# Optimization experiments

Measured on AMD Instinct MI355X. Metric: run time of the kernel, lower is better.

Reference implementation:

```python
import jax, jax.numpy as jnp
import numpy as np
from jax import lax

KQ = 3  # kernel_size_q
KK = 3  # kernel_size_k
PAD_Q = KQ - 1          # causal (left-only) padding along query dim
PAD_K = (KK - 1) // 2   # centered padding along key dim
CAUSAL = True


def setup_inputs() -> dict:
    key = jax.random.key(0)
    kq, kk, kv, kc = jax.random.split(key, 4)
    B, H, S, D = 1, 16, 2048, 128
    Q = jax.random.normal(kq, (B, H, S, D), dtype=jnp.float32)
    K = jax.random.normal(kk, (B, H, S, D), dtype=jnp.float32)
    V = jax.random.normal(kv, (B, H, S, D), dtype=jnp.float32)
    # module init: normal(mean=0, std=0.2)
    conv_kernel = 0.2 * jax.random.normal(kc, (H, KQ, KK), dtype=jnp.float32)
    return {"Q": Q, "K": K, "V": V, "conv_kernel": conv_kernel}


def reference(Q, K, V, conv_kernel):
    B, H, S, D = Q.shape
    scale = 1.0 / (D ** 0.5)
    # raw attention scores [B, H, Sq, Sk]
    scores = jnp.einsum('bhqd,bhkd->bhqk', Q, K) * scale
    causal_mask = jnp.tril(jnp.ones((S, S), dtype=bool))  # [Sq, Sk]
    if CAUSAL:
        # zero out future positions BEFORE the conv so the kernel cannot leak
        # future keys through the centered key-dim padding
        scores = jnp.where(causal_mask, scores, 0.0)
    # per-head 2D conv over the score matrix (grouped conv, one filter per head).
    # query dim padded only on the left (pad_q = KQ-1) -> each output row mixes
    # the current and previous KQ-1 query rows; key dim padded symmetrically.
    kernel = conv_kernel[:, None, :, :]  # [H, 1, KQ, KK] OIHW
    conv_scores = lax.conv_general_dilated(
        scores, kernel,
        window_strides=(1, 1),
        padding=[(PAD_Q, 0), (PAD_K, PAD_K)],
        dimension_numbers=('NCHW', 'OIHW', 'NCHW'),
        feature_group_count=H,
    )
    if CAUSAL:
        conv_scores = jnp.where(causal_mask, conv_scores, -jnp.inf)
    probs = jax.nn.softmax(conv_scores, axis=-1)
    out = jnp.einsum('bhqk,bhkd->bhqd', probs, V)
    return out
```

## Files before the change

kernel.cpp:

```cpp
#include <hip/hip_runtime.h>
#include <hip/hip_bf16.h>
#include <math.h>

#define S_LEN 2048
#define DIM   128
#define NHEAD 16
#define BQ    62
#define BK    64
#define SCALE 0.08838834764831845f

typedef __attribute__((ext_vector_type(8))) short bf16x8;
typedef __attribute__((ext_vector_type(4))) float f32x4;
typedef __attribute__((ext_vector_type(2))) float f32x2;

__device__ __forceinline__ short f2bf(float f) {
  union { float f; unsigned u; } v; v.f = f;
  unsigned r = v.u + 0x7fffu + ((v.u >> 16) & 1u);
  return (short)(r >> 16);
}
__device__ __forceinline__ float bhi(unsigned u) {
  union { unsigned v; float f; } x; x.v = u & 0xffff0000u; return x.f;
}
__device__ __forceinline__ float blo(unsigned u) {
  union { unsigned v; float f; } x; x.v = u << 16; return x.f;
}
__device__ __forceinline__ float b2f(short s) {
  union { unsigned v; float f; } x; x.v = ((unsigned)(unsigned short)s) << 16; return x.f;
}
__device__ __forceinline__ unsigned cvtpk(float lo, float hi) {
  unsigned r;
  asm("v_cvt_pk_bf16_f32 %0, %1, %2" : "=v"(r) : "v"(lo), "v"(hi));
  return r;
}
__device__ __forceinline__ f32x2 pkfma(f32x2 a, f32x2 b, f32x2 c) {
  f32x2 d;
  asm("v_pk_fma_f32 %0, %1, %2, %3" : "=v"(d) : "v"(a), "v"(b), "v"(c));
  return d;
}
__device__ __forceinline__ void gll16(const void* gsrc, void* ldst) {
  __builtin_amdgcn_global_load_lds(
      (const __attribute__((address_space(1))) void*)gsrc,
      (__attribute__((address_space(3))) void*)ldst, 16, 0, 0);
}

__global__ __launch_bounds__(256)
void prep_k(const float* __restrict__ K, short* __restrict__ Kb) {
  int gid = blockIdx.x * 256 + threadIdx.x;
  int chunk = gid & 15;
  int row = gid >> 4;
  int k = row & (S_LEN - 1);
  const float* src = K + (size_t)row * DIM + chunk * 8;
  float4 a = *(const float4*)(src);
  float4 b = *(const float4*)(src + 4);
  bf16x8 o;
  o[0]=f2bf(a.x*SCALE); o[1]=f2bf(a.y*SCALE); o[2]=f2bf(a.z*SCALE); o[3]=f2bf(a.w*SCALE);
  o[4]=f2bf(b.x*SCALE); o[5]=f2bf(b.y*SCALE); o[6]=f2bf(b.z*SCALE); o[7]=f2bf(b.w*SCALE);
  int cp = (chunk & 8) | ((chunk & 7) ^ (k & 7));
  *(bf16x8*)(Kb + (size_t)row * DIM + cp * 8) = o;
}

__global__ __launch_bounds__(256)
void prep_v(const float* __restrict__ V, short* __restrict__ Vw) {
  __shared__ __align__(16) short lv[128][72];
  int tile = blockIdx.x, h = blockIdx.y;
  const float* src = V + ((size_t)h * S_LEN + tile * 64) * DIM;
  int kr = threadIdx.x >> 2, dq = (threadIdx.x & 3) * 32;
  const float* sp = src + (size_t)kr * DIM + dq;
  #pragma unroll
  for (int j = 0; j < 32; j += 4) {
    float4 v = *(const float4*)(sp + j);
    lv[dq + j][kr]     = f2bf(v.x);
    lv[dq + j + 1][kr] = f2bf(v.y);
    lv[dq + j + 2][kr] = f2bf(v.z);
    lv[dq + j + 3][kr] = f2bf(v.w);
  }
  __syncthreads();
  int d = threadIdx.x >> 1, cbase = (threadIdx.x & 1) * 4;
  short* dst = Vw + ((size_t)h * 32 + tile) * 8192 + (size_t)d * 64;
  #pragma unroll
  for (int c0 = 0; c0 < 4; ++c0) {
    int c = cbase + c0;
    bf16x8 val = *(const bf16x8*)&lv[d][c * 8];
    *(bf16x8*)(dst + ((c ^ (d & 7)) * 8)) = val;
  }
}

__global__ __launch_bounds__(256, 2)
void convattn_main(const float* __restrict__ Q, const short* __restrict__ Kb,
                   const short* __restrict__ Vw, const float* __restrict__ W,
                   float* __restrict__ Out) {
  __shared__ __align__(16) short Kt2[2][64][128];
  __shared__ __align__(16) short Vt[128][64];
  __shared__ __align__(16) short rawS16[2][64][66];
  __shared__ short haloL16[2][64];

  const int bx = blockIdx.x;
  const int rank = (bx < 256) ? bx : ((bx < 512) ? (767 - bx) : bx);
  const int qt = 33 - (rank >> 4);
  const int h  = rank & 15;
  const int q0 = qt * BQ;
  const int qr0 = q0 - 2;
  const int q_cap = min(q0 + BQ - 1, S_LEN - 1);
  const int T = q_cap / BK + 1;

  const int tid  = threadIdx.x;
  const int wid  = tid >> 6;
  const int lane = tid & 63;
  const int lm   = lane & 15;
  const int lg   = lane >> 4;

  const float* Qh = Q + (size_t)h * S_LEN * DIM;
  const short* KbH = Kb + (size_t)h * S_LEN * DIM;
  const short* VwH = Vw + (size_t)h * 32 * 8192;
  float* Oh = Out + (size_t)h * S_LEN * DIM;

  f32x2 wp[9];
  #pragma unroll
  for (int i = 0; i < 9; ++i) { float w = W[h * 9 + i]; wp[i][0] = w; wp[i][1] = w; }

  bf16x8 qf[4];
  {
    int qrow = qr0 + wid * 16 + lm;
    int qc = qrow < 0 ? 0 : (qrow >= S_LEN ? S_LEN - 1 : qrow);
    const float* qp = Qh + (size_t)qc * DIM;
    #pragma unroll
    for (int kk = 0; kk < 4; ++kk) {
      int d0 = kk * 32 + lg * 8;
      float4 a = *(const float4*)(qp + d0);
      float4 b = *(const float4*)(qp + d0 + 4);
      bf16x8 f;
      f[0]=f2bf(a.x); f[1]=f2bf(a.y); f[2]=f2bf(a.z); f[3]=f2bf(a.w);
      f[4]=f2bf(b.x); f[5]=f2bf(b.y); f[6]=f2bf(b.z); f[7]=f2bf(b.w);
      qf[kk] = f;
    }
  }
  if (tid < 64) haloL16[0][tid] = 0;

  float m_state = -INFINITY, l_state = 0.f;
  f32x4 oacc[8];
  const f32x4 zero4 = {0.f, 0.f, 0.f, 0.f};
  #pragma unroll
  for (int cb = 0; cb < 8; ++cb) oacc[cb] = zero4;

  __builtin_amdgcn_sched_barrier(0);
  asm volatile("s_waitcnt vmcnt(0)" ::: "memory");
  {
    const char* vg = (const char*)VwH;
    const char* kg = (const char*)KbH;
    char* vl = (char*)&Vt[0][0];
    char* kl = (char*)&Kt2[0][0][0];
    #pragma unroll
    for (int i = 0; i < 4; ++i) {
      int off = wid * 4096 + i * 1024;
      gll16(vg + off + lane * 16, vl + off);
    }
    #pragma unroll
    for (int i = 0; i < 4; ++i) {
      int off = wid * 4096 + i * 1024;
      gll16(kg + off + lane * 16, kl + off);
    }
  }

  for (int t = 0; t <= T; ++t) {
    asm volatile("s_waitcnt lgkmcnt(0)" ::: "memory");
    __builtin_amdgcn_sched_barrier(0);
    __builtin_amdgcn_s_barrier();
    {
      int vsrc = t > 0 ? t - 1 : 0;
      int ksrc = (t + 1 < T) ? t + 1 : T - 1;
      const char* vg = (const char*)(VwH + (size_t)vsrc * 8192);
      const char* kg = (const char*)(KbH + (size_t)ksrc * BK * DIM);
      char* vl = (char*)&Vt[0][0];
      char* kl = (char*)&Kt2[(t + 1) & 1][0][0];
      #pragma unroll
      for (int i = 0; i < 4; ++i) {
        int off = wid * 4096 + i * 1024;
        gll16(vg + off + lane * 16, vl + off);
      }
      #pragma unroll
      for (int i = 0; i < 4; ++i) {
        int off = wid * 4096 + i * 1024;
        gll16(kg + off + lane * 16, kl + off);
      }
    }
    asm volatile("s_waitcnt vmcnt(8)" ::: "memory");
    __builtin_amdgcn_sched_barrier(0);
    __builtin_amdgcn_s_barrier();
    if (t < T) {
      const short(*Ktile)[128] = Kt2[t & 1];
      int k0 = t * BK;
      f32x4 sacc[4];
      #pragma unroll
      for (int cb = 0; cb < 4; ++cb) sacc[cb] = zero4;
      #pragma unroll
      for (int kk = 0; kk < 4; ++kk) {
        #pragma unroll
        for (int cb = 0; cb < 4; ++cb) {
          int c = kk * 4 + lg;
          int cp = (c & 8) | ((c & 7) ^ (lm & 7));
          bf16x8 bf = *(const bf16x8*)((const char*)&Ktile[cb * 16 + lm][0] + cp * 16);
          sacc[cb] = __builtin_amdgcn_mfma_f32_16x16x32_bf16(qf[kk], bf, sacc[cb], 0, 0, 0);
        }
      }
      const int buf = t & 1;
      #pragma unroll
      for (int cb = 0; cb < 4; ++cb) {
        int rr = wid * 16 + lg * 4;
        int cc = cb * 16 + lm;
        #pragma unroll
        for (int i = 0; i < 4; i += 2) {
          float v0 = ((k0 + cc) <= (qr0 + rr + i))     ? sacc[cb][i]     : 0.f;
          float v1 = ((k0 + cc) <= (qr0 + rr + i + 1)) ? sacc[cb][i + 1] : 0.f;
          unsigned pk = cvtpk(v0, v1);
          rawS16[buf][rr + i][cc]     = (short)pk;
          rawS16[buf][rr + i + 1][cc] = (short)(pk >> 16);
        }
      }
    }
    asm volatile("s_waitcnt vmcnt(4) lgkmcnt(0)" ::: "memory");
    __builtin_amdgcn_sched_barrier(0);
    __builtin_amdgcn_s_barrier();
    if (t > 0) {
      const int tp = t - 1;
      const int pb = tp & 1, nb = pb ^ 1;
      const int c0p = tp * BK;
      const bool haveRight = (t < T);
      const int r = wid * 16 + lm;
      const int q = qr0 + r;
      const bool rowvalid = (r >= 2) && (q <= q_cap);
      const int a0 = max(r - 2, 0), a1 = max(r - 1, 0);
      const short* rp[3] = { &rawS16[pb][a0][0], &rawS16[pb][a1][0], &rawS16[pb][r][0] };
      const int ridx[3] = { a0, a1, r };
      const int cs0 = lg * 8;
      const int cs1 = 32 + lg * 8;
      const bool leftEdge  = (lg == 0);
      const bool rightEdge = (lg == 3);
      const int cA = leftEdge ? 0 : cs0 - 2;

      f32x2 xv[3][10];
      #pragma unroll
      for (int rw = 0; rw < 3; ++rw) {
        const short* p = rp[rw];
        unsigned a0w = *(const unsigned*)(p + cA);
        unsigned a1w = *(const unsigned*)(p + cs0);
        unsigned a2w = *(const unsigned*)(p + cs0 + 2);
        unsigned a3w = *(const unsigned*)(p + cs0 + 4);
        unsigned a4w = *(const unsigned*)(p + cs0 + 6);
        unsigned a5w = *(const unsigned*)(p + cs0 + 8);
        unsigned b0w = *(const unsigned*)(p + cs1 - 2);
        unsigned b1w = *(const unsigned*)(p + cs1);
        unsigned b2w = *(const unsigned*)(p + cs1 + 2);
        unsigned b3w = *(const unsigned*)(p + cs1 + 4);
        unsigned b4w = *(const unsigned*)(p + cs1 + 6);
        unsigned b5w = *(const unsigned*)(p + cs1 + 8);
        float hv = b2f(haloL16[pb][ridx[rw]]);
        float rv = haveRight ? b2f(rawS16[nb][ridx[rw]][0]) : 0.f;
        xv[rw][0][0] = leftEdge ? hv : bhi(a0w);  xv[rw][0][1] = bhi(b0w);
        xv[rw][1][0] = blo(a1w);  xv[rw][1][1] = blo(b1w);
        xv[rw][2][0] = bhi(a1w);  xv[rw][2][1] = bhi(b1w);
        xv[rw][3][0] = blo(a2w);  xv[rw][3][1] = blo(b2w);
        xv[rw][4][0] = bhi(a2w);  xv[rw][4][1] = bhi(b2w);
        xv[rw][5][0] = blo(a3w);  xv[rw][5][1] = blo(b3w);
        xv[rw][6][0] = bhi(a3w);  xv[rw][6][1] = bhi(b3w);
        xv[rw][7][0] = blo(a4w);  xv[rw][7][1] = blo(b4w);
        xv[rw][8][0] = bhi(a4w);  xv[rw][8][1] = bhi(b4w);
        xv[rw][9][0] = blo(a5w);  xv[rw][9][1] = rightEdge ? rv : blo(b5w);
      }

      const int thr0 = rowvalid ? (q - c0p - cs0) : -1;
      const int thr1 = rowvalid ? (q - c0p - cs1) : -1;
      float svx[8], svy[8];
      float pm = -INFINITY;
      #pragma unroll
      for (int c = 0; c < 8; ++c) {
        f32x2 acc = {0.f, 0.f};
        acc = pkfma(wp[0], xv[0][c],     acc);
        acc = pkfma(wp[1], xv[0][c + 1], acc);
        acc = pkfma(wp[2], xv[0][c + 2], acc);
        acc = pkfma(wp[3], xv[1][c],     acc);
        acc = pkfma(wp[4], xv[1][c + 1], acc);
        acc = pkfma(wp[5], xv[1][c + 2], acc);
        acc = pkfma(wp[6], xv[2][c],     acc);
        acc = pkfma(wp[7], xv[2][c + 1], acc);
        acc = pkfma(wp[8], xv[2][c + 2], acc);
        svx[c] = (c <= thr0) ? acc[0] : -INFINITY;
        svy[c] = (c <= thr1) ? acc[1] : -INFINITY;
        pm = fmaxf(pm, fmaxf(svx[c], svy[c]));
      }
      pm = fmaxf(pm, __shfl_xor(pm, 16));
      pm = fmaxf(pm, __shfl_xor(pm, 32));
      const float mn = fmaxf(m_state, pm);
      const float al = __expf(m_state - mn);
      float ps = 0.f;
      union { bf16x8 v; unsigned u[4]; } pf0u, pf1u;
      #pragma unroll
      for (int c = 0; c < 8; c += 2) {
        float p0 = __expf(svx[c] - mn);
        float p1 = __expf(svx[c + 1] - mn);
        float p2 = __expf(svy[c] - mn);
        float p3 = __expf(svy[c + 1] - mn);
        ps += (p0 + p1) + (p2 + p3);
        pf0u.u[c >> 1] = cvtpk(p0, p1);
        pf1u.u[c >> 1] = cvtpk(p2, p3);
      }
      ps += __shfl_xor(ps, 16);
      ps += __shfl_xor(ps, 32);
      m_state = mn;
      l_state = al * l_state + ps;
      if (lg == 0) haloL16[t & 1][r] = rawS16[pb][r][63];
      #pragma unroll
      for (int i = 0; i < 4; ++i) {
        float a = __shfl(al, lg * 4 + i);
        #pragma unroll
        for (int cb = 0; cb < 8; ++cb) oacc[cb][i] *= a;
      }
      #pragma unroll
      for (int kk = 0; kk < 2; ++kk) {
        bf16x8 pf = kk ? pf1u.v : pf0u.v;
        #pragma unroll
        for (int cb = 0; cb < 8; ++cb) {
          int d = cb * 16 + lm;
          int cp = (kk * 4 + lg) ^ (lm & 7);
          bf16x8 vf = *(const bf16x8*)((const char*)&Vt[d][0] + cp * 16);
          oacc[cb] = __builtin_amdgcn_mfma_f32_16x16x32_bf16(pf, vf, oacc[cb], 0, 0, 0);
        }
      }
    }
  }

  asm volatile("s_waitcnt vmcnt(0)" ::: "memory");

  #pragma unroll
  for (int i = 0; i < 4; ++i) {
    int rr = wid * 16 + lg * 4 + i;
    int q = qr0 + rr;
    float lr = __shfl(l_state, lg * 4 + i);
    if (rr >= 2 && q <= q_cap) {
      float inv = 1.f / lr;
      #pragma unroll
      for (int cb = 0; cb < 8; ++cb) {
        Oh[(size_t)q * DIM + cb * 16 + lm] = oacc[cb][i] * inv;
      }
    }
  }
}

extern "C" void kernel_launch(void* const* d_in, const int* in_sizes, int n_in,
                              void* d_out, int out_size, void* d_ws, size_t ws_size,
                              hipStream_t stream) {
  const float* Q = (const float*)d_in[0];
  const float* K = (const float*)d_in[1];
  const float* V = (const float*)d_in[2];
  const float* W = (const float*)d_in[3];
  float* Out = (float*)d_out;
  short* Kb = (short*)d_ws;
  short* Vw = (short*)((char*)d_ws + (size_t)NHEAD * S_LEN * DIM * 2);

  prep_k<<<dim3(NHEAD * S_LEN * 16 / 256), 256, 0, stream>>>(K, Kb);
  prep_v<<<dim3(32, NHEAD), 256, 0, stream>>>(V, Vw);

  convattn_main<<<dim3(544), 256, 0, stream>>>(Q, Kb, Vw, W, Out);
}
```

Before: 104.2 us.

## Read K and V MFMA fragments directly from global memory instead of LDS staging

Removes the async global-to-LDS double-buffered staging of K and V tiles and the XOR swizzles in the prep kernels. The MFMA operands are now loaded straight from global (L2/L1-cached) bf16 buffers, and the custom waitcnt/barrier pipeline becomes plain __syncthreads. LDS use drops, and launch bounds are raised to 4 blocks per SM for more occupancy. The cost is that the tile loads are no longer overlapped with compute through prefetch, and every wave rereads K and V from global memory.

New measurement: 263.0 us. 152% more time.

```diff
diff --git a/kernel.cpp b/kernel.cpp
--- a/kernel.cpp
+++ b/kernel.cpp
@@ -37,26 +37,19 @@
   asm("v_pk_fma_f32 %0, %1, %2, %3" : "=v"(d) : "v"(a), "v"(b), "v"(c));
   return d;
 }
-__device__ __forceinline__ void gll16(const void* gsrc, void* ldst) {
-  __builtin_amdgcn_global_load_lds(
-      (const __attribute__((address_space(1))) void*)gsrc,
-      (__attribute__((address_space(3))) void*)ldst, 16, 0, 0);
-}
 
 __global__ __launch_bounds__(256)
 void prep_k(const float* __restrict__ K, short* __restrict__ Kb) {
   int gid = blockIdx.x * 256 + threadIdx.x;
   int chunk = gid & 15;
   int row = gid >> 4;
-  int k = row & (S_LEN - 1);
   const float* src = K + (size_t)row * DIM + chunk * 8;
   float4 a = *(const float4*)(src);
   float4 b = *(const float4*)(src + 4);
   bf16x8 o;
   o[0]=f2bf(a.x*SCALE); o[1]=f2bf(a.y*SCALE); o[2]=f2bf(a.z*SCALE); o[3]=f2bf(a.w*SCALE);
   o[4]=f2bf(b.x*SCALE); o[5]=f2bf(b.y*SCALE); o[6]=f2bf(b.z*SCALE); o[7]=f2bf(b.w*SCALE);
-  int cp = (chunk & 8) | ((chunk & 7) ^ (k & 7));
-  *(bf16x8*)(Kb + (size_t)row * DIM + cp * 8) = o;
+  *(bf16x8*)(Kb + (size_t)row * DIM + chunk * 8) = o;
 }
 
 __global__ __launch_bounds__(256)
@@ -64,15 +57,15 @@
   __shared__ __align__(16) short lv[128][72];
   int tile = blockIdx.x, h = blockIdx.y;
   const float* src = V + ((size_t)h * S_LEN + tile * 64) * DIM;
-  int kr = threadIdx.x >> 2, dq = (threadIdx.x & 3) * 32;
-  const float* sp = src + (size_t)kr * DIM + dq;
+  int kr = threadIdx.x >> 2, dc = (threadIdx.x & 3) * 32;
+  const float* sp = src + (size_t)kr * DIM + dc;
   #pragma unroll
   for (int j = 0; j < 32; j += 4) {
     float4 v = *(const float4*)(sp + j);
-    lv[dq + j][kr]     = f2bf(v.x);
-    lv[dq + j + 1][kr] = f2bf(v.y);
-    lv[dq + j + 2][kr] = f2bf(v.z);
-    lv[dq + j + 3][kr] = f2bf(v.w);
+    lv[dc + j][kr]     = f2bf(v.x);
+    lv[dc + j + 1][kr] = f2bf(v.y);
+    lv[dc + j + 2][kr] = f2bf(v.z);
+    lv[dc + j + 3][kr] = f2bf(v.w);
   }
   __syncthreads();
   int d = threadIdx.x >> 1, cbase = (threadIdx.x & 1) * 4;
@@ -80,17 +73,14 @@
   #pragma unroll
   for (int c0 = 0; c0 < 4; ++c0) {
     int c = cbase + c0;
-    bf16x8 val = *(const bf16x8*)&lv[d][c * 8];
-    *(bf16x8*)(dst + ((c ^ (d & 7)) * 8)) = val;
-  }
-}
-
-__global__ __launch_bounds__(256, 2)
+    *(bf16x8*)(dst + c * 8) = *(const bf16x8*)&lv[d][c * 8];
+  }
+}
+
+__global__ __launch_bounds__(256, 4)
 void convattn_main(const float* __restrict__ Q, const short* __restrict__ Kb,
-                   const short* __restrict__ Vw, const float* __restrict__ W,
+                   const short* __restrict__ Vw, const float* __restrict__ Wt,
                    float* __restrict__ Out) {
-  __shared__ __align__(16) short Kt2[2][64][128];
-  __shared__ __align__(16) short Vt[128][64];
   __shared__ __align__(16) short rawS16[2][64][66];
   __shared__ short haloL16[2][64];
 
@@ -116,7 +106,7 @@
 
   f32x2 wp[9];
   #pragma unroll
-  for (int i = 0; i < 9; ++i) { float w = W[h * 9 + i]; wp[i][0] = w; wp[i][1] = w; }
+  for (int i = 0; i < 9; ++i) { float w = Wt[h * 9 + i]; wp[i][0] = w; wp[i][1] = w; }
 
   bf16x8 qf[4];
   {
@@ -142,52 +132,9 @@
   #pragma unroll
   for (int cb = 0; cb < 8; ++cb) oacc[cb] = zero4;
 
-  __builtin_amdgcn_sched_barrier(0);
-  asm volatile("s_waitcnt vmcnt(0)" ::: "memory");
-  {
-    const char* vg = (const char*)VwH;
-    const char* kg = (const char*)KbH;
-    char* vl = (char*)&Vt[0][0];
-    char* kl = (char*)&Kt2[0][0][0];
-    #pragma unroll
-    for (int i = 0; i < 4; ++i) {
-      int off = wid * 4096 + i * 1024;
-      gll16(vg + off + lane * 16, vl + off);
-    }
-    #pragma unroll
-    for (int i = 0; i < 4; ++i) {
-      int off = wid * 4096 + i * 1024;
-      gll16(kg + off + lane * 16, kl + off);
-    }
-  }
-
   for (int t = 0; t <= T; ++t) {
-    asm volatile("s_waitcnt lgkmcnt(0)" ::: "memory");
-    __builtin_amdgcn_sched_barrier(0);
-    __builtin_amdgcn_s_barrier();
-    {
-      int vsrc = t > 0 ? t - 1 : 0;
-      int ksrc = (t + 1 < T) ? t + 1 : T - 1;
-      const char* vg = (const char*)(VwH + (size_t)vsrc * 8192);
-      const char* kg = (const char*)(KbH + (size_t)ksrc * BK * DIM);
-      char* vl = (char*)&Vt[0][0];
-      char* kl = (char*)&Kt2[(t + 1) & 1][0][0];
-      #pragma unroll
-      for (int i = 0; i < 4; ++i) {
-        int off = wid * 4096 + i * 1024;
-        gll16(vg + off + lane * 16, vl + off);
-      }
-      #pragma unroll
-      for (int i = 0; i < 4; ++i) {
-        int off = wid * 4096 + i * 1024;
-        gll16(kg + off + lane * 16, kl + off);
-      }
-    }
-    asm volatile("s_waitcnt vmcnt(8)" ::: "memory");
-    __builtin_amdgcn_sched_barrier(0);
-    __builtin_amdgcn_s_barrier();
+    __syncthreads();
     if (t < T) {
-      const short(*Ktile)[128] = Kt2[t & 1];
       int k0 = t * BK;
       f32x4 sacc[4];
       #pragma unroll
@@ -196,9 +143,8 @@
       for (int kk = 0; kk < 4; ++kk) {
         #pragma unroll
         for (int cb = 0; cb < 4; ++cb) {
-          int c = kk * 4 + lg;
-          int cp = (c & 8) | ((c & 7) ^ (lm & 7));
-          bf16x8 bf = *(const bf16x8*)((const char*)&Ktile[cb * 16 + lm][0] + cp * 16);
+          const short* kp = KbH + (size_t)(k0 + cb * 16 + lm) * DIM + (kk * 4 + lg) * 8;
+          bf16x8 bf = *(const bf16x8*)kp;
           sacc[cb] = __builtin_amdgcn_mfma_f32_16x16x32_bf16(qf[kk], bf, sacc[cb], 0, 0, 0);
         }
       }
@@ -217,9 +163,7 @@
         }
       }
     }
-    asm volatile("s_waitcnt vmcnt(4) lgkmcnt(0)" ::: "memory");
-    __builtin_amdgcn_sched_barrier(0);
-    __builtin_amdgcn_s_barrier();
+    __syncthreads();
     if (t > 0) {
       const int tp = t - 1;
       const int pb = tp & 1, nb = pb ^ 1;
@@ -314,21 +258,19 @@
         #pragma unroll
         for (int cb = 0; cb < 8; ++cb) oacc[cb][i] *= a;
       }
+      const short* Vtile = VwH + (size_t)tp * 8192;
       #pragma unroll
       for (int kk = 0; kk < 2; ++kk) {
         bf16x8 pf = kk ? pf1u.v : pf0u.v;
         #pragma unroll
         for (int cb = 0; cb < 8; ++cb) {
-          int d = cb * 16 + lm;
-          int cp = (kk * 4 + lg) ^ (lm & 7);
-          bf16x8 vf = *(const bf16x8*)((const char*)&Vt[d][0] + cp * 16);
+          const short* vp = Vtile + (size_t)(cb * 16 + lm) * 64 + (kk * 4 + lg) * 8;
+          bf16x8 vf = *(const bf16x8*)vp;
           oacc[cb] = __builtin_amdgcn_mfma_f32_16x16x32_bf16(pf, vf, oacc[cb], 0, 0, 0);
         }
       }
     }
   }
-
-  asm volatile("s_waitcnt vmcnt(0)" ::: "memory");
 
   #pragma unroll
   for (int i = 0; i < 4; ++i) {
@@ -353,10 +295,11 @@
   const float* V = (const float*)d_in[2];
   const float* W = (const float*)d_in[3];
   float* Out = (float*)d_out;
+
   short* Kb = (short*)d_ws;
-  short* Vw = (short*)((char*)d_ws + (size_t)NHEAD * S_LEN * DIM * 2);
-
-  prep_k<<<dim3(NHEAD * S_LEN * 16 / 256), 256, 0, stream>>>(K, Kb);
+  short* Vw = (short*)((char*)d_ws + 8388608);
+
+  prep_k<<<dim3(2048), 256, 0, stream>>>(K, Kb);
   prep_v<<<dim3(32, NHEAD), 256, 0, stream>>>(V, Vw);
 
   convattn_main<<<dim3(544), 256, 0, stream>>>(Q, Kb, Vw, W, Out);
```

## Read V fragments directly from global memory and stage fp32 scores in LDS

Applied to the files above, without the earlier changes.

The V tile is no longer staged in LDS through global_load_lds. The PV MFMA B operands are now read straight from the pre-transposed bf16 V workspace in global/L2, and prep_v drops its XOR swizzle to match. The raw score tile is kept in LDS as fp32 with an interleaved column layout instead of packed bf16, so the conv reads float2 pairs directly without unpacking. s_setprio is raised around both MFMA loops. The changes save LDS space and barrier-coupled traffic, but V reads now take per-iteration global latency on the critical path and the LDS score buffer doubles in size.

Result: slower. 159.2 us (+52.7%).

```diff
diff --git a/kernel.cpp b/kernel.cpp
--- a/kernel.cpp
+++ b/kernel.cpp
@@ -17,15 +17,6 @@
   union { float f; unsigned u; } v; v.f = f;
   unsigned r = v.u + 0x7fffu + ((v.u >> 16) & 1u);
   return (short)(r >> 16);
-}
-__device__ __forceinline__ float bhi(unsigned u) {
-  union { unsigned v; float f; } x; x.v = u & 0xffff0000u; return x.f;
-}
-__device__ __forceinline__ float blo(unsigned u) {
-  union { unsigned v; float f; } x; x.v = u << 16; return x.f;
-}
-__device__ __forceinline__ float b2f(short s) {
-  union { unsigned v; float f; } x; x.v = ((unsigned)(unsigned short)s) << 16; return x.f;
 }
 __device__ __forceinline__ unsigned cvtpk(float lo, float hi) {
   unsigned r;
@@ -64,15 +55,15 @@
   __shared__ __align__(16) short lv[128][72];
   int tile = blockIdx.x, h = blockIdx.y;
   const float* src = V + ((size_t)h * S_LEN + tile * 64) * DIM;
-  int kr = threadIdx.x >> 2, dq = (threadIdx.x & 3) * 32;
-  const float* sp = src + (size_t)kr * DIM + dq;
+  int kr = threadIdx.x >> 2, dc = (threadIdx.x & 3) * 32;
+  const float* sp = src + (size_t)kr * DIM + dc;
   #pragma unroll
   for (int j = 0; j < 32; j += 4) {
     float4 v = *(const float4*)(sp + j);
-    lv[dq + j][kr]     = f2bf(v.x);
-    lv[dq + j + 1][kr] = f2bf(v.y);
-    lv[dq + j + 2][kr] = f2bf(v.z);
-    lv[dq + j + 3][kr] = f2bf(v.w);
+    lv[dc + j][kr]     = f2bf(v.x);
+    lv[dc + j + 1][kr] = f2bf(v.y);
+    lv[dc + j + 2][kr] = f2bf(v.z);
+    lv[dc + j + 3][kr] = f2bf(v.w);
   }
   __syncthreads();
   int d = threadIdx.x >> 1, cbase = (threadIdx.x & 1) * 4;
@@ -80,19 +71,17 @@
   #pragma unroll
   for (int c0 = 0; c0 < 4; ++c0) {
     int c = cbase + c0;
-    bf16x8 val = *(const bf16x8*)&lv[d][c * 8];
-    *(bf16x8*)(dst + ((c ^ (d & 7)) * 8)) = val;
+    *(bf16x8*)(dst + c * 8) = *(const bf16x8*)&lv[d][c * 8];
   }
 }
 
 __global__ __launch_bounds__(256, 2)
 void convattn_main(const float* __restrict__ Q, const short* __restrict__ Kb,
-                   const short* __restrict__ Vw, const float* __restrict__ W,
+                   const short* __restrict__ Vw, const float* __restrict__ Wt,
                    float* __restrict__ Out) {
   __shared__ __align__(16) short Kt2[2][64][128];
-  __shared__ __align__(16) short Vt[128][64];
-  __shared__ __align__(16) short rawS16[2][64][66];
-  __shared__ short haloL16[2][64];
+  __shared__ __align__(16) float rawF[2][64][70];
+  __shared__ float haloLF[2][64];
 
   const int bx = blockIdx.x;
   const int rank = (bx < 256) ? bx : ((bx < 512) ? (767 - bx) : bx);
@@ -116,7 +105,7 @@
 
   f32x2 wp[9];
   #pragma unroll
-  for (int i = 0; i < 9; ++i) { float w = W[h * 9 + i]; wp[i][0] = w; wp[i][1] = w; }
+  for (int i = 0; i < 9; ++i) { float w = Wt[h * 9 + i]; wp[i][0] = w; wp[i][1] = w; }
 
   bf16x8 qf[4];
   {
@@ -134,7 +123,7 @@
       qf[kk] = f;
     }
   }
-  if (tid < 64) haloL16[0][tid] = 0;
+  if (tid < 64) haloLF[0][tid] = 0.f;
 
   float m_state = -INFINITY, l_state = 0.f;
   f32x4 oacc[8];
@@ -144,20 +133,12 @@
 
   __builtin_amdgcn_sched_barrier(0);
   asm volatile("s_waitcnt vmcnt(0)" ::: "memory");
+  __builtin_amdgcn_sched_barrier(0);
   {
-    const char* vg = (const char*)VwH;
-    const char* kg = (const char*)KbH;
-    char* vl = (char*)&Vt[0][0];
-    char* kl = (char*)&Kt2[0][0][0];
     #pragma unroll
     for (int i = 0; i < 4; ++i) {
       int off = wid * 4096 + i * 1024;
-      gll16(vg + off + lane * 16, vl + off);
-    }
-    #pragma unroll
-    for (int i = 0; i < 4; ++i) {
-      int off = wid * 4096 + i * 1024;
-      gll16(kg + off + lane * 16, kl + off);
+      gll16((const char*)KbH + off + lane * 16, (char*)&Kt2[0][0][0] + off);
     }
   }
 
@@ -166,24 +147,16 @@
     __builtin_amdgcn_sched_barrier(0);
     __builtin_amdgcn_s_barrier();
     {
-      int vsrc = t > 0 ? t - 1 : 0;
       int ksrc = (t + 1 < T) ? t + 1 : T - 1;
-      const char* vg = (const char*)(VwH + (size_t)vsrc * 8192);
       const char* kg = (const char*)(KbH + (size_t)ksrc * BK * DIM);
-      char* vl = (char*)&Vt[0][0];
       char* kl = (char*)&Kt2[(t + 1) & 1][0][0];
-      #pragma unroll
-      for (int i = 0; i < 4; ++i) {
-        int off = wid * 4096 + i * 1024;
-        gll16(vg + off + lane * 16, vl + off);
-      }
       #pragma unroll
       for (int i = 0; i < 4; ++i) {
         int off = wid * 4096 + i * 1024;
         gll16(kg + off + lane * 16, kl + off);
       }
     }
-    asm volatile("s_waitcnt vmcnt(8)" ::: "memory");
+    asm volatile("s_waitcnt vmcnt(4)" ::: "memory");
     __builtin_amdgcn_sched_barrier(0);
     __builtin_amdgcn_s_barrier();
     if (t < T) {
@@ -192,6 +165,7 @@
       f32x4 sacc[4];
       #pragma unroll
       for (int cb = 0; cb < 4; ++cb) sacc[cb] = zero4;
+      __builtin_amdgcn_s_setprio(1);
       #pragma unroll
       for (int kk = 0; kk < 4; ++kk) {
         #pragma unroll
@@ -202,22 +176,21 @@
           sacc[cb] = __builtin_amdgcn_mfma_f32_16x16x32_bf16(qf[kk], bf, sacc[cb], 0, 0, 0);
         }
       }
+      __builtin_amdgcn_s_setprio(0);
       const int buf = t & 1;
       #pragma unroll
       for (int cb = 0; cb < 4; ++cb) {
         int rr = wid * 16 + lg * 4;
         int cc = cb * 16 + lm;
-        #pragma unroll
-        for (int i = 0; i < 4; i += 2) {
-          float v0 = ((k0 + cc) <= (qr0 + rr + i))     ? sacc[cb][i]     : 0.f;
-          float v1 = ((k0 + cc) <= (qr0 + rr + i + 1)) ? sacc[cb][i + 1] : 0.f;
-          unsigned pk = cvtpk(v0, v1);
-          rawS16[buf][rr + i][cc]     = (short)pk;
-          rawS16[buf][rr + i + 1][cc] = (short)(pk >> 16);
-        }
-      }
-    }
-    asm volatile("s_waitcnt vmcnt(4) lgkmcnt(0)" ::: "memory");
+        int di = ((cc & 31) + 2) * 2 + (cc >> 5);
+        #pragma unroll
+        for (int i = 0; i < 4; ++i) {
+          float v = ((k0 + cc) <= (qr0 + rr + i)) ? sacc[cb][i] : 0.f;
+          rawF[buf][rr + i][di] = v;
+        }
+      }
+    }
+    asm volatile("s_waitcnt lgkmcnt(0)" ::: "memory");
     __builtin_amdgcn_sched_barrier(0);
     __builtin_amdgcn_s_barrier();
     if (t > 0) {
@@ -229,42 +202,34 @@
       const int q = qr0 + r;
       const bool rowvalid = (r >= 2) && (q <= q_cap);
       const int a0 = max(r - 2, 0), a1 = max(r - 1, 0);
-      const short* rp[3] = { &rawS16[pb][a0][0], &rawS16[pb][a1][0], &rawS16[pb][r][0] };
       const int ridx[3] = { a0, a1, r };
+      const f32x2* rp[3] = { (const f32x2*)&rawF[pb][a0][0],
+                             (const f32x2*)&rawF[pb][a1][0],
+                             (const f32x2*)&rawF[pb][r][0] };
       const int cs0 = lg * 8;
       const int cs1 = 32 + lg * 8;
-      const bool leftEdge  = (lg == 0);
-      const bool rightEdge = (lg == 3);
-      const int cA = leftEdge ? 0 : cs0 - 2;
+      const int jb = lg * 8 + 1;
 
       f32x2 xv[3][10];
       #pragma unroll
       for (int rw = 0; rw < 3; ++rw) {
-        const short* p = rp[rw];
-        unsigned a0w = *(const unsigned*)(p + cA);
-        unsigned a1w = *(const unsigned*)(p + cs0);
-        unsigned a2w = *(const unsigned*)(p + cs0 + 2);
-        unsigned a3w = *(const unsigned*)(p + cs0 + 4);
-        unsigned a4w = *(const unsigned*)(p + cs0 + 6);
-        unsigned a5w = *(const unsigned*)(p + cs0 + 8);
-        unsigned b0w = *(const unsigned*)(p + cs1 - 2);
-        unsigned b1w = *(const unsigned*)(p + cs1);
-        unsigned b2w = *(const unsigned*)(p + cs1 + 2);
-        unsigned b3w = *(const unsigned*)(p + cs1 + 4);
-        unsigned b4w = *(const unsigned*)(p + cs1 + 6);
-        unsigned b5w = *(const unsigned*)(p + cs1 + 8);
-        float hv = b2f(haloL16[pb][ridx[rw]]);
-        float rv = haveRight ? b2f(rawS16[nb][ridx[rw]][0]) : 0.f;
-        xv[rw][0][0] = leftEdge ? hv : bhi(a0w);  xv[rw][0][1] = bhi(b0w);
-        xv[rw][1][0] = blo(a1w);  xv[rw][1][1] = blo(b1w);
-        xv[rw][2][0] = bhi(a1w);  xv[rw][2][1] = bhi(b1w);
-        xv[rw][3][0] = blo(a2w);  xv[rw][3][1] = blo(b2w);
-        xv[rw][4][0] = bhi(a2w);  xv[rw][4][1] = bhi(b2w);
-        xv[rw][5][0] = blo(a3w);  xv[rw][5][1] = blo(b3w);
-        xv[rw][6][0] = bhi(a3w);  xv[rw][6][1] = bhi(b3w);
-        xv[rw][7][0] = blo(a4w);  xv[rw][7][1] = blo(b4w);
-        xv[rw][8][0] = bhi(a4w);  xv[rw][8][1] = bhi(b4w);
-        xv[rw][9][0] = blo(a5w);  xv[rw][9][1] = rightEdge ? rv : blo(b5w);
+        #pragma unroll
+        for (int i = 0; i < 10; ++i) xv[rw][i] = rp[rw][jb + i];
+      }
+      if (lg == 0) {
+        #pragma unroll
+        for (int rw = 0; rw < 3; ++rw) {
+          xv[rw][0][0] = haloLF[pb][ridx[rw]];
+          xv[rw][0][1] = rp[rw][33][0];
+        }
+      }
+      if (lg == 3) {
+        #pragma unroll
+        for (int rw = 0; rw < 3; ++rw) {
+          xv[rw][9][0] = rp[rw][2][1];
+          xv[rw][9][1] = haveRight
+              ? ((const f32x2*)&rawF[nb][ridx[rw]][0])[2][0] : 0.f;
+        }
       }
 
       const int thr0 = rowvalid ? (q - c0p - cs0) : -1;
@@ -307,24 +272,26 @@
       ps += __shfl_xor(ps, 32);
       m_state = mn;
       l_state = al * l_state + ps;
-      if (lg == 0) haloL16[t & 1][r] = rawS16[pb][r][63];
+      if (lg == 0) haloLF[t & 1][r] = rawF[pb][r][67];
       #pragma unroll
       for (int i = 0; i < 4; ++i) {
         float a = __shfl(al, lg * 4 + i);
         #pragma unroll
         for (int cb = 0; cb < 8; ++cb) oacc[cb][i] *= a;
       }
+      const short* Vtile = VwH + (size_t)tp * 8192;
+      __builtin_amdgcn_s_setprio(1);
       #pragma unroll
       for (int kk = 0; kk < 2; ++kk) {
         bf16x8 pf = kk ? pf1u.v : pf0u.v;
         #pragma unroll
         for (int cb = 0; cb < 8; ++cb) {
-          int d = cb * 16 + lm;
-          int cp = (kk * 4 + lg) ^ (lm & 7);
-          bf16x8 vf = *(const bf16x8*)((const char*)&Vt[d][0] + cp * 16);
+          const short* vp = Vtile + (size_t)(cb * 16 + lm) * 64 + (kk * 4 + lg) * 8;
+          bf16x8 vf = *(const bf16x8*)vp;
           oacc[cb] = __builtin_amdgcn_mfma_f32_16x16x32_bf16(pf, vf, oacc[cb], 0, 0, 0);
         }
       }
+      __builtin_amdgcn_s_setprio(0);
     }
   }
 
@@ -353,10 +320,11 @@
   const float* V = (const float*)d_in[2];
   const float* W = (const float*)d_in[3];
   float* Out = (float*)d_out;
+
   short* Kb = (short*)d_ws;
-  short* Vw = (short*)((char*)d_ws + (size_t)NHEAD * S_LEN * DIM * 2);
-
-  prep_k<<<dim3(NHEAD * S_LEN * 16 / 256), 256, 0, stream>>>(K, Kb);
+  short* Vw = (short*)((char*)d_ws + 8388608);
+
+  prep_k<<<dim3(2048), 256, 0, stream>>>(K, Kb);
   prep_v<<<dim3(32, NHEAD), 256, 0, stream>>>(V, Vw);
 
   convattn_main<<<dim3(544), 256, 0, stream>>>(Q, Kb, Vw, W, Out);
```
